# Kernel tuning notes

Hardware: AMD Instinct MI355X
Metric: run time of the kernel (lower is better)

## Reference

```python
import jax, jax.numpy as jnp
import numpy as np

K_NN = 3
T = 100
D = 50
BS = 2
CH = 100  # must equal T for the cat in forward to be valid
RES_INNER = 12
RES_CTX = 16
EXPAND = 0.5


def make_anchors(bs, t, d):
    S, Du = np.meshgrid(np.arange(t), np.arange(d), indexing='ij')  # [t, d]
    valid = (S + Du) < t
    cl = (Du + 1).astype(np.float32)
    xmin = np.where(valid, S - cl * EXPAND, 0.0).astype(np.float32)
    xmax = np.where(valid, S + Du + cl * EXPAND, 0.0).astype(np.float32)
    per = np.stack([xmin.reshape(-1), xmax.reshape(-1)], axis=1)  # [t*d, 2]
    rows = []
    for k in range(bs):
        b = np.full((per.shape[0], 1), float(k), dtype=np.float32)
        rows.append(np.concatenate([b, per], axis=1))
    return np.concatenate(rows, axis=0)  # [bs*t*d, 3]


def align1d(feat, rois, resolution):
    # feat: [B, C, L], rois: [N, 3] = (batch_idx, start, end) -> [N, C, resolution]
    B, C, L = feat.shape
    b = rois[:, 0].astype(jnp.int32)
    start, end = rois[:, 1], rois[:, 2]
    bin_w = (end - start) / resolution                       # [N]
    offs = (jnp.arange(resolution, dtype=feat.dtype) + 0.5)  # [R]
    coords = start[:, None] + offs[None, :] * bin_w[:, None] # [N, R]
    valid = (coords >= -1.0) & (coords <= L)                 # zero outside roi support
    lo = jnp.floor(coords)
    frac = coords - lo
    lo_i = jnp.clip(lo.astype(jnp.int32), 0, L - 1)
    hi_i = jnp.clip(lo_i + 1, 0, L - 1)
    flat = feat.transpose(0, 2, 1).reshape(B * L, C)         # [B*L, C]
    base = b[:, None] * L                                    # [N, 1]
    v_lo = flat[base + lo_i]                                 # [N, R, C]
    v_hi = flat[base + hi_i]
    vals = v_lo * (1.0 - frac[..., None]) + v_hi * frac[..., None]
    vals = jnp.where(valid[..., None], vals, 0.0)
    return vals.transpose(0, 2, 1)                           # [N, C, R]


def knn_idx(x, k):
    # x: [B, C, T]; faithful to source (uses x**3, not x**2)
    inner = -2.0 * jnp.einsum('bct,bcs->bts', x, x)          # [B, T, T]
    xx = jnp.sum(x ** 3, axis=1, keepdims=True)              # [B, 1, T]
    pd = -xx - inner - jnp.swapaxes(xx, 1, 2)                # [B, T, T]
    _, idx = jax.lax.top_k(pd, k)                            # [B, T, k]
    return idx


def setup_inputs() -> dict:
    key = jax.random.key(0)
    kx, = jax.random.split(key, 1)
    x = jax.random.normal(kx, (BS, CH, T), dtype=jnp.float32)
    anchors = jnp.asarray(make_anchors(BS, T, D))
    index = jnp.zeros((BS,), dtype=jnp.int64)
    return {'x': x, 'anchors': anchors, 'index': index}


def reference(x, anchors, index):
    bs, ch, t = x.shape
    anchor = anchors[: T * D * bs, :]                        # [N, 3]
    feat_inner = align1d(x, anchor, RES_INNER)               # [N, ch, 12]
    # get_graph_feature(x, k=3, style=2): gather k-NN neighbor features
    idx = knn_idx(x, K_NN)                                   # [bs, t, k]
    xT = x.transpose(0, 2, 1)                                # [bs, t, ch]
    b_ar = jnp.arange(bs)[:, None, None]
    feature = xT[b_ar, idx]                                  # [bs, t, k, ch]
    ctx = feature.mean(axis=-1)                              # [bs, t, k] (mean over dims, per source)
    feat_context = align1d(ctx, anchor, RES_CTX)             # [N, t, 16]
    feat = jnp.concatenate([feat_inner, feat_context], axis=2)  # [N, ch, 28] (needs ch == t)
    feat = feat.reshape(bs, t, D, -1)                        # [bs, t, d, ch*28]
    return feat.transpose(0, 3, 2, 1)                        # [bs, ch*28, d, t]
```

## Files before the change

### kernel.cpp

```cpp
#include <hip/hip_runtime.h>
#include <math.h>

#define T_   100
#define D_   50
#define BS_  2
#define CH_  100
#define RI_  12
#define RC_  16
#define KNN_ 3
#define NJ_  (RI_ + RC_)
#define QD_  (CH_ * NJ_)
#define TOTAL_ (BS_ * QD_ * D_ * T_)

#define CT_  10
#define XP_  104

__global__ __launch_bounds__(128) void ctx_kernel(const float* __restrict__ x,
                                                  float* __restrict__ ctx) {
    __shared__ float xs[CH_ * T_];
    __shared__ float cm[T_];
    __shared__ float va[128];

    const int b = blockIdx.x / T_;
    const int t = blockIdx.x - b * T_;
    const float* xb = x + b * CH_ * T_;

    const float4* xb4 = (const float4*)xb;
    float4* xs4 = (float4*)xs;
    for (int i = threadIdx.x; i < (CH_ * T_) / 4; i += 128) xs4[i] = xb4[i];
    __syncthreads();

    const int s = threadIdx.x;
    float v = -INFINITY;
    if (s < T_) {
        float dot = 0.f, cube = 0.f, colsum = 0.f;
        #pragma unroll 4
        for (int c = 0; c < CH_; ++c) {
            float vv = xs[c * T_ + s];
            float vt = xs[c * T_ + t];
            dot    += vv * vt;
            cube   += vv * vv * vv;
            colsum += vv;
        }
        v = 2.f * dot - cube;
        cm[s] = colsum * (1.0f / (float)CH_);
    }
    va[threadIdx.x] = v;
    __syncthreads();

    if (threadIdx.x < 64) {
        const int l = threadIdx.x;
        const float c0v = va[l];
        const float c1v = va[l + 64];
        int sel0 = -100, sel1 = -100;
        for (int k = 0; k < KNN_; ++k) {
            float v0 = (l == sel0 || l == sel1) ? -INFINITY : c0v;
            float v1 = (l + 64 == sel0 || l + 64 == sel1) ? -INFINITY : c1v;
            float bv; int bi;
            if (v1 > v0) { bv = v1; bi = l + 64; } else { bv = v0; bi = l; }
            #pragma unroll
            for (int off = 32; off > 0; off >>= 1) {
                float ov = __shfl_xor(bv, off);
                int   oi = __shfl_xor(bi, off);
                if (ov > bv || (ov == bv && oi < bi)) { bv = ov; bi = oi; }
            }
            if (l == 0) ctx[(b * T_ + t) * KNN_ + k] = cm[bi];
            if (k == 0) sel0 = bi; else sel1 = bi;
        }
    }
}

__global__ __launch_bounds__(256) void out_kernel(const float* __restrict__ x,
                                                  const float* __restrict__ anchors,
                                                  const float* __restrict__ ctx,
                                                  float* __restrict__ out) {
    __shared__ float an_s[T_], an_e[T_];
    __shared__ alignas(16) float frac_a[NJ_ * T_];
    __shared__ alignas(16) int   lo_a[NJ_ * T_];
    __shared__ float xs[CT_ * XP_];
    __shared__ float cs[CT_ * 4];

    const int nct = CH_ / CT_;
    const int ct  = blockIdx.x % nct;
    const int du  = (blockIdx.x / nct) % D_;
    const int b   = blockIdx.x / (nct * D_);
    const int c0  = ct * CT_;
    const int tid = threadIdx.x;

    if (tid < T_) {
        int r = (b * T_ + tid) * D_ + du;
        an_s[tid] = anchors[3 * r + 1];
        an_e[tid] = anchors[3 * r + 2];
    }
    const float* xg = x + (b * CH_ + c0) * T_;
    for (int i = tid; i < CT_ * T_; i += 256) {
        int cl = i / T_, ss = i - cl * T_;
        xs[cl * XP_ + ss] = xg[i];
    }
    if (tid < CT_) xs[tid * XP_ + T_] = xg[tid * T_ + (T_ - 1)];
    if (tid < CT_) {
        const float* cg = ctx + (b * T_ + c0 + tid) * KNN_;
        cs[tid * 4 + 0] = cg[0];
        cs[tid * 4 + 1] = cg[1];
        cs[tid * 4 + 2] = cg[2];
        cs[tid * 4 + 3] = cg[2];
    }
    __syncthreads();

    for (int p = tid; p < NJ_ * T_; p += 256) {
        int j = p / T_;
        int s = p - j * T_;
        bool inner = j < RI_;
        float jsc = inner ? ((float)j + 0.5f) * (1.0f / (float)RI_)
                          : ((float)(j - RI_) + 0.5f) * (1.0f / (float)RC_);
        float st = an_s[s], en = an_e[s];
        float coord = st + jsc * (en - st);
        float Lf  = inner ? (float)T_ : (float)KNN_;
        int   Lm1 = inner ? (T_ - 1) : (KNN_ - 1);
        bool valid = (coord >= -1.0f) && (coord <= Lf);
        float lof = floorf(coord);
        int lo = (int)lof;
        lo = lo < 0 ? 0 : (lo > Lm1 ? Lm1 : lo);
        frac_a[p] = coord - lof;
        lo_a[p]   = valid ? lo : -1;
    }
    __syncthreads();

    for (int e4 = tid; e4 < CT_ * NJ_ * (T_ / 4); e4 += 256) {
        int cl  = e4 / (NJ_ * (T_ / 4));
        int rem = e4 - cl * (NJ_ * (T_ / 4));
        int j   = rem / (T_ / 4);
        int s4  = rem - j * (T_ / 4);
        const float* fr = (j < RI_) ? &xs[cl * XP_] : &cs[cl * 4];
        int p = j * T_ + s4 * 4;
        float4 f4 = *(const float4*)&frac_a[p];
        int4   l4 = *(const int4*)&lo_a[p];
        int   lv[4] = {l4.x, l4.y, l4.z, l4.w};
        float fv[4] = {f4.x, f4.y, f4.z, f4.w};
        float res[4];
        #pragma unroll
        for (int i = 0; i < 4; ++i) {
            int le = lv[i];
            int lu = le < 0 ? 0 : le;
            float f = fv[i];
            float vv = fr[lu] * (1.0f - f) + fr[lu + 1] * f;
            res[i] = le < 0 ? 0.0f : vv;
        }
        float4 ov = make_float4(res[0], res[1], res[2], res[3]);
        *(float4*)(out + ((((b * QD_ + (c0 + cl) * NJ_ + j) * D_) + du) * T_ + s4 * 4)) = ov;
    }
}

extern "C" void kernel_launch(void* const* d_in, const int* in_sizes, int n_in,
                              void* d_out, int out_size, void* d_ws, size_t ws_size,
                              hipStream_t stream) {
    const float* x       = (const float*)d_in[0];
    const float* anchors = (const float*)d_in[1];
    float* ctx = (float*)d_ws;
    float* out = (float*)d_out;

    ctx_kernel<<<BS_ * T_, 128, 0, stream>>>(x, ctx);

    const int blocks = BS_ * D_ * (CH_ / CT_);
    out_kernel<<<blocks, 256, 0, stream>>>(x, anchors, ctx, out);
}
```

Measured before the change: 149.3 us.

## Compute interpolation coords in registers and reuse across channels in out_kernel

out_kernel no longer builds shared-memory frac/lo tables in a separate pass. Each thread now owns one (j, 4-position) slot, computes its coordinates, weights and masks once in registers, and reuses them across a loop over the channel tile. This drops one barrier and the shared-memory round trip. The channel tile shrinks to 5, the block grows to 704 threads, and the x tile gets bank-conflict padding. ctx_kernel stops staging the whole 40KB input in shared memory and reads global memory directly with more unrolling, which lowers LDS use and may raise occupancy but leans on cache for the repeated column reads.

```diff
diff --git a/kernel.cpp b/kernel.cpp
--- a/kernel.cpp
+++ b/kernel.cpp
@@ -10,42 +10,34 @@
 #define KNN_ 3
 #define NJ_  (RI_ + RC_)
 #define QD_  (CH_ * NJ_)
-#define TOTAL_ (BS_ * QD_ * D_ * T_)
-
-#define CT_  10
-#define XP_  104
+#define CT_  5
+#define XPS_ 104
 
 __global__ __launch_bounds__(128) void ctx_kernel(const float* __restrict__ x,
                                                   float* __restrict__ ctx) {
-    __shared__ float xs[CH_ * T_];
     __shared__ float cm[T_];
     __shared__ float va[128];
 
     const int b = blockIdx.x / T_;
     const int t = blockIdx.x - b * T_;
     const float* xb = x + b * CH_ * T_;
+    const int s = threadIdx.x;
 
-    const float4* xb4 = (const float4*)xb;
-    float4* xs4 = (float4*)xs;
-    for (int i = threadIdx.x; i < (CH_ * T_) / 4; i += 128) xs4[i] = xb4[i];
-    __syncthreads();
-
-    const int s = threadIdx.x;
-    float v = -INFINITY;
+    float key = -INFINITY;
     if (s < T_) {
         float dot = 0.f, cube = 0.f, colsum = 0.f;
-        #pragma unroll 4
+        #pragma unroll 10
         for (int c = 0; c < CH_; ++c) {
-            float vv = xs[c * T_ + s];
-            float vt = xs[c * T_ + t];
+            float vv = xb[c * T_ + s];
+            float vt = xb[c * T_ + t];
             dot    += vv * vt;
             cube   += vv * vv * vv;
             colsum += vv;
         }
-        v = 2.f * dot - cube;
+        key = 2.f * dot - cube;
         cm[s] = colsum * (1.0f / (float)CH_);
     }
-    va[threadIdx.x] = v;
+    va[threadIdx.x] = key;
     __syncthreads();
 
     if (threadIdx.x < 64) {
@@ -70,14 +62,12 @@
     }
 }
 
-__global__ __launch_bounds__(256) void out_kernel(const float* __restrict__ x,
+__global__ __launch_bounds__(704) void out_kernel(const float* __restrict__ x,
                                                   const float* __restrict__ anchors,
                                                   const float* __restrict__ ctx,
                                                   float* __restrict__ out) {
     __shared__ float an_s[T_], an_e[T_];
-    __shared__ alignas(16) float frac_a[NJ_ * T_];
-    __shared__ alignas(16) int   lo_a[NJ_ * T_];
-    __shared__ float xs[CT_ * XP_];
+    __shared__ float xs[CT_ * XPS_];
     __shared__ float cs[CT_ * 4];
 
     const int nct = CH_ / CT_;
@@ -87,67 +77,71 @@
     const int c0  = ct * CT_;
     const int tid = threadIdx.x;
 
-    if (tid < T_) {
-        int r = (b * T_ + tid) * D_ + du;
-        an_s[tid] = anchors[3 * r + 1];
-        an_e[tid] = anchors[3 * r + 2];
+    if (tid < 2 * T_) {
+        int ss = tid >> 1, comp = tid & 1;
+        int r = (b * T_ + ss) * D_ + du;
+        float v = anchors[3 * r + 1 + comp];
+        if (comp) an_e[ss] = v; else an_s[ss] = v;
     }
-    const float* xg = x + (b * CH_ + c0) * T_;
-    for (int i = tid; i < CT_ * T_; i += 256) {
-        int cl = i / T_, ss = i - cl * T_;
-        xs[cl * XP_ + ss] = xg[i];
+    if (tid < CT_ * T_) {
+        int cl = tid / T_, ss = tid - cl * T_;
+        xs[cl * XPS_ + ss + (ss >> 5)] = x[(b * CH_ + c0 + cl) * T_ + ss];
     }
-    if (tid < CT_) xs[tid * XP_ + T_] = xg[tid * T_ + (T_ - 1)];
-    if (tid < CT_) {
-        const float* cg = ctx + (b * T_ + c0 + tid) * KNN_;
-        cs[tid * 4 + 0] = cg[0];
-        cs[tid * 4 + 1] = cg[1];
-        cs[tid * 4 + 2] = cg[2];
-        cs[tid * 4 + 3] = cg[2];
+    if (tid >= 512 && tid < 512 + CT_) {
+        int cl = tid - 512;
+        xs[cl * XPS_ + 103] = x[(b * CH_ + c0 + cl) * T_ + (T_ - 1)];
+    }
+    if (tid >= 520 && tid < 520 + CT_) {
+        int cl = tid - 520;
+        const float* cg = ctx + (b * T_ + c0 + cl) * KNN_;
+        cs[cl * 4 + 0] = cg[0];
+        cs[cl * 4 + 1] = cg[1];
+        cs[cl * 4 + 2] = cg[2];
+        cs[cl * 4 + 3] = cg[2];
     }
     __syncthreads();
 
-    for (int p = tid; p < NJ_ * T_; p += 256) {
-        int j = p / T_;
-        int s = p - j * T_;
-        bool inner = j < RI_;
-        float jsc = inner ? ((float)j + 0.5f) * (1.0f / (float)RI_)
-                          : ((float)(j - RI_) + 0.5f) * (1.0f / (float)RC_);
-        float st = an_s[s], en = an_e[s];
+    if (tid >= NJ_ * (T_ / 4)) return;
+    const int j  = tid / (T_ / 4);
+    const int s4 = tid - j * (T_ / 4);
+    const int s0 = s4 * 4;
+    const bool inner = (j < RI_);
+    const float jsc = inner ? ((float)j + 0.5f) * (1.0f / (float)RI_)
+                            : ((float)(j - RI_) + 0.5f) * (1.0f / (float)RC_);
+    const float Lf  = inner ? (float)T_ : (float)KNN_;
+    const int   Lm1 = inner ? (T_ - 1) : (KNN_ - 1);
+    const float* fb   = inner ? xs : cs;
+    const int rstride = inner ? XPS_ : 4;
+
+    int pl_[4], ph_[4];
+    float f_[4], msk[4];
+    #pragma unroll
+    for (int i = 0; i < 4; ++i) {
+        float st = an_s[s0 + i], en = an_e[s0 + i];
         float coord = st + jsc * (en - st);
-        float Lf  = inner ? (float)T_ : (float)KNN_;
-        int   Lm1 = inner ? (T_ - 1) : (KNN_ - 1);
-        bool valid = (coord >= -1.0f) && (coord <= Lf);
+        msk[i] = ((coord >= -1.0f) && (coord <= Lf)) ? 1.0f : 0.0f;
         float lof = floorf(coord);
+        f_[i] = coord - lof;
         int lo = (int)lof;
         lo = lo < 0 ? 0 : (lo > Lm1 ? Lm1 : lo);
-        frac_a[p] = coord - lof;
-        lo_a[p]   = valid ? lo : -1;
+        int hi = lo + 1;
+        pl_[i] = inner ? lo + (lo >> 5) : lo;
+        ph_[i] = inner ? hi + (hi >> 5) : hi;
     }
-    __syncthreads();
 
-    for (int e4 = tid; e4 < CT_ * NJ_ * (T_ / 4); e4 += 256) {
-        int cl  = e4 / (NJ_ * (T_ / 4));
-        int rem = e4 - cl * (NJ_ * (T_ / 4));
-        int j   = rem / (T_ / 4);
-        int s4  = rem - j * (T_ / 4);
-        const float* fr = (j < RI_) ? &xs[cl * XP_] : &cs[cl * 4];
-        int p = j * T_ + s4 * 4;
-        float4 f4 = *(const float4*)&frac_a[p];
-        int4   l4 = *(const int4*)&lo_a[p];
-        int   lv[4] = {l4.x, l4.y, l4.z, l4.w};
-        float fv[4] = {f4.x, f4.y, f4.z, f4.w};
+    int obase = (((b * QD_ + c0 * NJ_ + j) * D_) + du) * T_ + s0;
+    const int ostride = NJ_ * D_ * T_;
+    #pragma unroll
+    for (int cl = 0; cl < CT_; ++cl) {
+        const float* fr = fb + cl * rstride;
         float res[4];
         #pragma unroll
         for (int i = 0; i < 4; ++i) {
-            int le = lv[i];
-            int lu = le < 0 ? 0 : le;
-            float f = fv[i];
-            float vv = fr[lu] * (1.0f - f) + fr[lu + 1] * f;
-            res[i] = le < 0 ? 0.0f : vv;
+            float f = f_[i];
+            res[i] = (fr[pl_[i]] * (1.0f - f) + fr[ph_[i]] * f) * msk[i];
         }
-        float4 ov = make_float4(res[0], res[1], res[2], res[3]);
-        *(float4*)(out + ((((b * QD_ + (c0 + cl) * NJ_ + j) * D_) + du) * T_ + s4 * 4)) = ov;
+        *(float4*)(out + obase) = make_float4(res[0], res[1], res[2], res[3]);
+        obase += ostride;
     }
 }
 
@@ -162,5 +156,5 @@
     ctx_kernel<<<BS_ * T_, 128, 0, stream>>>(x, ctx);
 
     const int blocks = BS_ * D_ * (CH_ / CT_);
-    out_kernel<<<blocks, 256, 0, stream>>>(x, anchors, ctx, out);
+    out_kernel<<<blocks, 704, 0, stream>>>(x, anchors, ctx, out);
 }
```

After: 140.3 us. 6.0% less time.
